# Optimization experiments

Measured on AMD Instinct MI355X. Metric: run time of the kernel, lower is better.

Reference implementation:

```python
import math
import jax, jax.numpy as jnp
import numpy as np

L, F, K = 3, 128, 20          # layers, hidden size, rbf size
CUTOFF = 5.0
B, NPER, EPER = 4, 4096, 49152  # graphs, nodes/graph, edges/graph
NVOC = 119                    # len(ase.data.atomic_numbers)
PNAMES = ['atom_emb','pot_W','pot_b','init_W1','init_b1','init_W2','init_b2','vec_w',
          'filt_W','filt_b','msg_W1','msg_b1','msg_W2','msg_b2','U_W','V_W',
          'upd_W1','upd_b1','upd_W2','upd_b2']


def _painn(atom_xyz, cell, nodes, atom_edges, edges_displacement, V_flat, E_flat, p):
    N = B * NPER
    pos = atom_xyz.reshape(N, 3)
    # edge_offset = cumsum(num_nodes) ; all graphs have NPER nodes
    off = (jnp.arange(B, dtype=atom_edges.dtype) * NPER)[:, None, None]
    edges = (atom_edges + off).reshape(B * EPER, 2)
    # calc_distance with periodic cell offsets
    disp = jnp.einsum('bec,bcd->bed', edges_displacement, cell).reshape(B * EPER, 3)
    send, recv = edges[:, 0], edges[:, 1]
    diff = pos[recv] - (pos[send] + disp)                       # [E,3]
    dist = jnp.sqrt(jnp.sum(diff * diff, axis=1, keepdims=True))  # [E,1]
    # sinc RBF expansion
    n_range = jnp.arange(1, K + 1, dtype=jnp.float32)
    edge_state = jnp.sin(dist * n_range * (math.pi / CUTOFF)) / dist  # [E,K]
    # init scalar features: Embedding(Z) || Linear(V) -> MLP
    s_atom = p['atom_emb'][nodes.reshape(N)]                    # [N,F]
    s_pot = V_flat @ p['pot_W'].T + p['pot_b']                  # [N,F]
    h = jnp.concatenate([s_atom, s_pot], axis=-1)
    s = jax.nn.silu(h @ p['init_W1'].T + p['init_b1']) @ p['init_W2'].T + p['init_b2']  # [N,F]
    # init vector features: no-bias Linear(1->F) on E field
    v = E_flat[:, :, None] * p['vec_w']                         # [N,3,F]
    cut = jnp.where(dist < CUTOFF, 0.5 * (jnp.cos(math.pi * dist / CUTOFF) + 1.0), 0.0)  # [E,1]
    dirn = diff / jnp.maximum(dist, 1e-12)                      # [E,3]
    s_list, v_list = [], []
    for l in range(L):
        # --- PaiNNInteraction ---
        fw = (edge_state @ p['filt_W'][l].T + p['filt_b'][l]) * cut                # [E,3F]
        so = jax.nn.silu(s @ p['msg_W1'][l].T + p['msg_b1'][l]) @ p['msg_W2'][l].T + p['msg_b2'][l]  # [N,3F]
        fo = fw * so[send]                                                          # [E,3F]
        g_sv, g_ev, g_ns = jnp.split(fo, 3, axis=1)
        msg_s = s[send] * g_ns                                                      # [E,F]
        msg_v = v[send] * g_sv[:, None, :] + g_ev[:, None, :] * dirn[:, :, None]    # [E,3,F]
        s = s + jax.ops.segment_sum(msg_s, recv, num_segments=N)
        v = v + jax.ops.segment_sum(msg_v, recv, num_segments=N)
        # --- PaiNNUpdate ---
        Uv = v @ p['U_W'][l].T                                                      # [N,3,F]
        Vv = v @ p['V_W'][l].T                                                      # [N,3,F]
        Vn = jnp.sqrt(jnp.sum(Vv * Vv, axis=1))                                     # [N,F]
        m = jnp.concatenate([s, Vn], axis=1)
        m = jax.nn.silu(m @ p['upd_W1'][l].T + p['upd_b1'][l]) @ p['upd_W2'][l].T + p['upd_b2'][l]
        a_ss, a_sv, a_vv = jnp.split(m, 3, axis=1)
        s = s + a_ss + a_sv * jnp.sum(Uv * Vv, axis=1)
        v = v + a_vv[:, None, :] * Uv
        s_list.append(s)
        v_list.append(v)
    # pack trajectory: [L,N,1,F] scalar || [L,N,3,F] vector -> [L,N,4,F]
    return jnp.concatenate([jnp.stack(s_list)[:, :, None, :], jnp.stack(v_list)], axis=2)


def setup_inputs() -> dict:
    key = jax.random.key(0)
    ks = iter(jax.random.split(key, 48))
    def nrm(shape, scale=0.05):
        return jax.random.normal(next(ks), shape, dtype=jnp.float32) * scale
    atom_xyz = jax.random.uniform(next(ks), (B, NPER, 3), dtype=jnp.float32) * 30.0
    cell = jnp.tile(jnp.eye(3, dtype=jnp.float32)[None] * 30.0, (B, 1, 1))
    nodes = jax.random.randint(next(ks), (B, NPER), 0, NVOC)
    e0 = jax.random.randint(next(ks), (B, EPER), 0, NPER)
    delta = jax.random.randint(next(ks), (B, EPER), 1, NPER)
    e1 = (e0 + delta) % NPER  # sender != receiver -> no zero-distance edges
    atom_edges = jnp.stack([e0, e1], axis=-1)
    edges_displacement = jax.random.randint(next(ks), (B, EPER, 3), -1, 2).astype(jnp.float32)
    V_flat = nrm((B * NPER, 1), 1.0)
    E_flat = nrm((B * NPER, 3), 1.0)
    params = dict(
        atom_emb=nrm((NVOC, F), 1.0),
        pot_W=nrm((F, 1)), pot_b=nrm((F,)),
        init_W1=nrm((F, 2 * F)), init_b1=nrm((F,)),
        init_W2=nrm((F, F)), init_b2=nrm((F,)),
        vec_w=nrm((F,)),
        filt_W=nrm((L, 3 * F, K)), filt_b=nrm((L, 3 * F)),
        msg_W1=nrm((L, F, F)), msg_b1=nrm((L, F)),
        msg_W2=nrm((L, 3 * F, F)), msg_b2=nrm((L, 3 * F)),
        U_W=nrm((L, F, F)), V_W=nrm((L, F, F)),
        upd_W1=nrm((L, F, 2 * F)), upd_b1=nrm((L, F)),
        upd_W2=nrm((L, 3 * F, F)), upd_b2=nrm((L, 3 * F)),
    )
    return dict(atom_xyz=atom_xyz, cell=cell, nodes=nodes, atom_edges=atom_edges,
                edges_displacement=edges_displacement, V_flat=V_flat, E_flat=E_flat, **params)


def reference(atom_xyz, cell, nodes, atom_edges, edges_displacement, V_flat, E_flat,
              atom_emb, pot_W, pot_b, init_W1, init_b1, init_W2, init_b2, vec_w,
              filt_W, filt_b, msg_W1, msg_b1, msg_W2, msg_b2, U_W, V_W,
              upd_W1, upd_b1, upd_W2, upd_b2):
    p = dict(zip(PNAMES, (atom_emb, pot_W, pot_b, init_W1, init_b1, init_W2, init_b2, vec_w,
                          filt_W, filt_b, msg_W1, msg_b1, msg_W2, msg_b2, U_W, V_W,
                          upd_W1, upd_b1, upd_W2, upd_b2)))
    return _painn(atom_xyz, cell, nodes, atom_edges, edges_displacement, V_flat, E_flat, p)
```

## Files before the change

### kernel.cpp

```cpp
#include <hip/hip_runtime.h>
#include <math.h>

#define NPER  4096
#define NTOT  16384
#define EPER  49152
#define ETOT  196608
#define FD    128
#define F3    384
#define KR    20
#define PI_F  3.14159265358979f
#define PADF  132

typedef unsigned short u16;
typedef __attribute__((ext_vector_type(8))) short s16x8;
typedef __attribute__((ext_vector_type(4))) float f32x4;
typedef _Float16 h16x2 __attribute__((ext_vector_type(2)));
typedef _Float16 h16x4 __attribute__((ext_vector_type(4)));
typedef _Float16 h16x8 __attribute__((ext_vector_type(8)));

#if defined(__has_builtin)
#if __has_builtin(__builtin_amdgcn_fdot2)
#define FDOT2(a,b,c) __builtin_amdgcn_fdot2((a),(b),(c),false)
#endif
#endif
#ifndef FDOT2
#define FDOT2(a,b,c) ((float)(a)[0]*(float)(b)[0] + (float)(a)[1]*(float)(b)[1] + (c))
#endif

__device__ __forceinline__ float silu_f(float x){ return x / (1.0f + __expf(-x)); }
__device__ __forceinline__ u16 f2b(float x){
    unsigned u = __float_as_uint(x);
    u = u + 0x7FFFu + ((u >> 16) & 1u);
    return (u16)(u >> 16);
}
__device__ __forceinline__ float b2f(u16 h){ return __uint_as_float(((unsigned)h) << 16); }

struct __align__(16) EdgeRec {
    float4 ed;
    h16x8  es0;
    h16x8  es1;
    h16x4  es2;
    h16x4  pad;
};

__global__ __launch_bounds__(256) void ecount_kernel(
    const int* __restrict__ aedges, int* __restrict__ counts)
{
    int e = blockIdx.x * blockDim.x + threadIdx.x;
    if (e >= ETOT) return;
    int r = aedges[(size_t)e*2+1] + (e / EPER)*NPER;
    atomicAdd(&counts[r],1);
}

__global__ __launch_bounds__(1024) void scan_kernel(const int* __restrict__ counts,
                                                    int* __restrict__ row_off)
{
    __shared__ int sdata[1024];
    int t = threadIdx.x;
    int base = t * 16;
    int local[16];
    int s = 0;
    #pragma unroll
    for (int i=0;i<16;++i){ local[i]=s; s += counts[base+i]; }
    sdata[t] = s;
    __syncthreads();
    for (int off=1; off<1024; off<<=1) {
        int val = (t>=off) ? sdata[t-off] : 0;
        __syncthreads();
        sdata[t] += val;
        __syncthreads();
    }
    int chunk_off = (t==0) ? 0 : sdata[t-1];
    #pragma unroll
    for (int i=0;i<16;++i) row_off[base+i] = chunk_off + local[i];
    if (t==1023) row_off[NTOT] = sdata[1023];
}

__global__ __launch_bounds__(256) void fill_kernel(
    const float* __restrict__ xyz, const float* __restrict__ cell,
    const int* __restrict__ aedges, const float* __restrict__ edisp,
    const int* __restrict__ row_off, int* __restrict__ cursor,
    int* __restrict__ sd_csr, EdgeRec* __restrict__ erec_csr)
{
    int e = blockIdx.x * blockDim.x + threadIdx.x;
    if (e >= ETOT) return;
    int b = e / EPER;
    int s = aedges[(size_t)e*2+0] + b*NPER;
    int r = aedges[(size_t)e*2+1] + b*NPER;
    const float* cb = cell + b*9;
    float c0 = edisp[(size_t)e*3+0], c1 = edisp[(size_t)e*3+1], c2 = edisp[(size_t)e*3+2];
    float diff[3];
    #pragma unroll
    for (int d=0; d<3; ++d) {
        float disp = c0*cb[d] + c1*cb[3+d] + c2*cb[6+d];
        diff[d] = xyz[(size_t)r*3+d] - (xyz[(size_t)s*3+d] + disp);
    }
    float dist = sqrtf(diff[0]*diff[0]+diff[1]*diff[1]+diff[2]*diff[2]);
    float cut = (dist < 5.0f) ? 0.5f*(__cosf(PI_F*dist*0.2f)+1.0f) : 0.0f;
    float invg = 1.0f/fmaxf(dist,1e-12f);
    EdgeRec rec;
    rec.ed = make_float4(diff[0]*invg, diff[1]*invg, diff[2]*invg, cut);
    float theta = dist*(PI_F*0.2f);
    float s1 = __sinf(theta), cth = __cosf(theta);
    float scale = cut / dist;
    float twoc = 2.f*cth;
    float sm1 = 0.f, sk = s1;
    _Float16 esv[20];
    #pragma unroll
    for (int k=0;k<20;++k){
        esv[k] = (_Float16)(sk*scale);
        float nx = twoc*sk - sm1;
        sm1 = sk; sk = nx;
    }
    union { h16x8 v; _Float16 h[8]; } u0, u1;
    union { h16x4 v; _Float16 h[4]; } u2;
    #pragma unroll
    for (int i=0;i<8;++i){ u0.h[i]=esv[i]; u1.h[i]=esv[8+i]; }
    #pragma unroll
    for (int i=0;i<4;++i) u2.h[i]=esv[16+i];
    rec.es0=u0.v; rec.es1=u1.v; rec.es2=u2.v;
    rec.pad = (h16x4)((_Float16)0);
    int slot = atomicAdd(&cursor[r], 1);
    int pos = row_off[r] + slot;
    sd_csr[pos] = s;
    erec_csr[pos] = rec;
}

__global__ __launch_bounds__(256) void wconv_kernel(
    const float* __restrict__ w0, const float* __restrict__ w1,
    const float* __restrict__ w2, const float* __restrict__ w3,
    const float* __restrict__ w4, const float* __restrict__ w5,
    const float* __restrict__ w6, const float* __restrict__ w7,
    u16* __restrict__ dst)
{
    int t = blockIdx.x*256 + threadIdx.x;
    if (t >= 589824) return;
    const float* src; int off; int d = t;
    if      (t < 32768)  { src=w0; off=t; }
    else if (t < 49152)  { src=w1; off=t-32768; }
    else if (t < 98304)  { src=w2; off=t-49152; }
    else if (t < 245760) { src=w3; off=t-98304; }
    else if (t < 294912) { int o=t-245760; int l=o>>14; int r=o&16383; src=w4; off=o;
                           d = 245760 + l*32768 + r; }
    else if (t < 344064) { int o=t-294912; int l=o>>14; int r=o&16383; src=w5; off=o;
                           d = 245760 + l*32768 + 16384 + r; }
    else if (t < 442368) { src=w6; off=t-344064; }
    else                 { src=w7; off=t-442368; }
    dst[d] = f2b(src[off]);
}

__global__ __launch_bounds__(256) void wfilt_kernel(const float* __restrict__ fW,
                                                    _Float16* __restrict__ dst)
{
    int t = blockIdx.x*256 + threadIdx.x;
    if (t < 3*F3*KR) dst[t] = (_Float16)fW[t];
}

__global__ __launch_bounds__(256) void hbuild_kernel(const int* __restrict__ nodes,
    const float* __restrict__ atom_emb, const float* __restrict__ V_flat,
    const float* __restrict__ pot_W, const float* __restrict__ pot_b,
    u16* __restrict__ h)
{
    int t = blockIdx.x * blockDim.x + threadIdx.x;
    int n = t >> 8, k = t & 255;
    float val;
    if (k < FD) val = atom_emb[(size_t)nodes[n]*FD + k];
    else { int f = k - FD; val = V_flat[n]*pot_W[f] + pot_b[f]; }
    h[t] = f2b(val);
}

__global__ __launch_bounds__(256) void v0_kernel(const float* __restrict__ E_flat,
    const float* __restrict__ vec_w, float* __restrict__ v0, u16* __restrict__ vq)
{
    int t = blockIdx.x * blockDim.x + threadIdx.x;
    int n = t / F3, r = t - n*F3;
    int c = r >> 7, f = r & 127;
    float val = E_flat[(size_t)n*3 + c] * vec_w[f];
    v0[t] = val;
    vq[((size_t)n*FD + f)*4 + c] = f2b(val);
}

template<int ACT>
__global__ __launch_bounds__(256) void bgemm_kernel(
    const u16* __restrict__ A, int lda,
    const u16* __restrict__ W, int Kdim,
    const float* __restrict__ bias,
    float* __restrict__ C, int ldc,
    u16* __restrict__ Cb, int ldcb,
    u16* __restrict__ Cq, int qoff)
{
    const int tid  = threadIdx.x;
    const int wave = tid >> 6, lane = tid & 63;
    const int q = lane >> 4, im = lane & 15;
    const int row0 = blockIdx.y*64 + wave*16;
    const int col0 = blockIdx.x*64;
    f32x4 acc[4];
    #pragma unroll
    for (int n=0;n<4;++n) acc[n] = (f32x4){0.f,0.f,0.f,0.f};
    const u16* Ap = A + (size_t)(row0+im)*lda + q*8;
    const u16* Wp = W + (size_t)(col0+im)*Kdim + q*8;
    for (int k0 = 0; k0 < Kdim; k0 += 32) {
        s16x8 af = *(const s16x8*)(Ap + k0);
        #pragma unroll
        for (int n=0;n<4;++n) {
            s16x8 bf = *(const s16x8*)(Wp + (size_t)n*16*Kdim + k0);
            acc[n] = __builtin_amdgcn_mfma_f32_16x16x32_bf16(af, bf, acc[n], 0, 0, 0);
        }
    }
    #pragma unroll
    for (int n=0;n<4;++n) {
        int col = col0 + n*16 + im;
        float bv = bias ? bias[col] : 0.f;
        #pragma unroll
        for (int r=0;r<4;++r) {
            int row = row0 + q*4 + r;
            float v = acc[n][r] + bv;
            if (ACT) v = silu_f(v);
            if (C)  C[(size_t)row*ldc + col] = v;
            if (Cb) Cb[(size_t)row*ldcb + col] = f2b(v);
            if (Cq) Cq[((size_t)row*FD + (col & 127))*4 + (col >> 7) + qoff] = f2b(v);
        }
    }
}

#define HID_OFF(row, col2b) ((unsigned)((row)*256 + (col2b)*2) ^ ((unsigned)((row)&7) << 4))
#define M_OFF(row, col2b)   ((unsigned)((row)*512 + (col2b)*2) ^ ((unsigned)((row)&7) << 4))

__global__ __launch_bounds__(256) void msgmlp_kernel(
    const u16* __restrict__ A,
    const u16* __restrict__ W1,
    const float* __restrict__ b1,
    const u16* __restrict__ W2,
    const float* __restrict__ b2,
    u16* __restrict__ sq)
{
    __shared__ u16 hid[16*FD];
    const int tid = threadIdx.x;
    const int wave = tid >> 6, lane = tid & 63;
    const int q = lane >> 4, im = lane & 15;
    const int row0 = blockIdx.x * 16;
    {
        f32x4 acc[2];
        #pragma unroll
        for (int n=0;n<2;++n) acc[n] = (f32x4){0.f,0.f,0.f,0.f};
        const u16* Ap = A + (size_t)(row0+im)*FD + q*8;
        #pragma unroll
        for (int k0=0;k0<FD;k0+=32) {
            s16x8 af = *(const s16x8*)(Ap + k0);
            #pragma unroll
            for (int n=0;n<2;++n) {
                s16x8 bf = *(const s16x8*)(W1 + (size_t)(wave*32+n*16+im)*FD + k0 + q*8);
                acc[n] = __builtin_amdgcn_mfma_f32_16x16x32_bf16(af, bf, acc[n], 0, 0, 0);
            }
        }
        #pragma unroll
        for (int n=0;n<2;++n) {
            int col = wave*32 + n*16 + im;
            float bv = b1[col];
            #pragma unroll
            for (int r=0;r<4;++r) {
                int row = q*4 + r;
                *(u16*)((char*)hid + HID_OFF(row, col)) = f2b(silu_f(acc[n][r]+bv));
            }
        }
    }
    __syncthreads();
    s16x8 af[4];
    #pragma unroll
    for (int k=0;k<4;++k)
        af[k] = *(const s16x8*)((char*)hid + HID_OFF(im, k*32+q*8));
    #pragma unroll
    for (int jj=0;jj<2;++jj) {
        int j = wave*2 + jj;
        f32x4 a2[3];
        #pragma unroll
        for (int g=0;g<3;++g) a2[g] = (f32x4){0.f,0.f,0.f,0.f};
        #pragma unroll
        for (int k=0;k<4;++k) {
            #pragma unroll
            for (int g=0;g<3;++g) {
                s16x8 bf = *(const s16x8*)(W2 + (size_t)(g*128 + j*16 + im)*FD + k*32 + q*8);
                a2[g] = __builtin_amdgcn_mfma_f32_16x16x32_bf16(af[k], bf, a2[g], 0, 0, 0);
            }
        }
        int fcol = j*16 + im;
        float c0 = b2[fcol], c1 = b2[FD+fcol], c2 = b2[2*FD+fcol];
        #pragma unroll
        for (int r=0;r<4;++r) {
            int row = row0 + q*4 + r;
            size_t t4 = ((size_t)row*FD + fcol)*4;
            unsigned pk = (unsigned)f2b(a2[0][r]+c0) | ((unsigned)f2b(a2[1][r]+c1) << 16);
            *(unsigned*)(sq + t4) = pk;
            sq[t4+2] = f2b(a2[2][r]+c2);
        }
    }
}

__global__ __launch_bounds__(256) void upduv_kernel(
    const u16* __restrict__ vmid4,
    const u16* __restrict__ Wuv,
    const u16* __restrict__ W1,
    const float* __restrict__ b1,
    const u16* __restrict__ W2,
    const float* __restrict__ b2,
    const float* __restrict__ s_mid, const float* __restrict__ v_mid,
    float* __restrict__ outp, u16* __restrict__ s_bf,
    u16* __restrict__ sq, u16* __restrict__ vq)
{
    __shared__ u16   mL[16*256];
    __shared__ float dotL[16*PADF];
    __shared__ float uvL[48*PADF];
    __shared__ u16   hid[16*FD];
    const int tid = threadIdx.x;
    const int wave = tid >> 6, lane = tid & 63;
    const int q = lane >> 4, im = lane & 15;
    const int node0 = blockIdx.x * 16;

    {
        const int prow0 = blockIdx.x*64 + wave*16;
        const u16* Ap = vmid4 + (size_t)(prow0+im)*FD + q*8;
        s16x8 af[4];
        #pragma unroll
        for (int k=0;k<4;++k) af[k] = *(const s16x8*)(Ap + k*32);
        const int nloc = wave*4 + q;
        #pragma unroll
        for (int j=0;j<8;++j) {
            f32x4 aU = (f32x4){0.f,0.f,0.f,0.f};
            f32x4 aV = (f32x4){0.f,0.f,0.f,0.f};
            const u16* WpU = Wuv + (size_t)(j*16+im)*FD + q*8;
            const u16* WpV = WpU + (size_t)128*FD;
            #pragma unroll
            for (int k=0;k<4;++k) {
                s16x8 bU = *(const s16x8*)(WpU + k*32);
                s16x8 bV = *(const s16x8*)(WpV + k*32);
                aU = __builtin_amdgcn_mfma_f32_16x16x32_bf16(af[k], bU, aU, 0, 0, 0);
                aV = __builtin_amdgcn_mfma_f32_16x16x32_bf16(af[k], bV, aV, 0, 0, 0);
            }
            int fcol = j*16 + im;
            float u0=aU[0], u1=aU[1], u2=aU[2];
            float w0=aV[0], w1=aV[1], w2=aV[2];
            dotL[nloc*PADF + fcol] = u0*w0 + u1*w1 + u2*w2;
            *(u16*)((char*)mL + M_OFF(nloc, 128+fcol)) = f2b(sqrtf(w0*w0+w1*w1+w2*w2));
            uvL[(nloc*3+0)*PADF + fcol] = u0;
            uvL[(nloc*3+1)*PADF + fcol] = u1;
            uvL[(nloc*3+2)*PADF + fcol] = u2;
        }
    }
    {
        int row = tid >> 4;
        int c0  = (tid & 15) * 8;
        const float* sp = s_mid + (size_t)(node0+row)*FD + c0;
        union { s16x8 v; u16 h[8]; } pk;
        #pragma unroll
        for (int i=0;i<8;++i) pk.h[i] = f2b(sp[i]);
        *(s16x8*)((char*)mL + M_OFF(row, c0)) = pk.v;
    }
    __syncthreads();
    {
        f32x4 acc[2];
        #pragma unroll
        for (int n=0;n<2;++n) acc[n] = (f32x4){0.f,0.f,0.f,0.f};
        #pragma unroll
        for (int k0=0;k0<256;k0+=32) {
            s16x8 af = *(const s16x8*)((char*)mL + M_OFF(im, k0+q*8));
            #pragma unroll
            for (int n=0;n<2;++n) {
                s16x8 bf = *(const s16x8*)(W1 + (size_t)(wave*32+n*16+im)*256 + k0 + q*8);
                acc[n] = __builtin_amdgcn_mfma_f32_16x16x32_bf16(af, bf, acc[n], 0, 0, 0);
            }
        }
        #pragma unroll
        for (int n=0;n<2;++n) {
            int col = wave*32 + n*16 + im;
            float bv = b1[col];
            #pragma unroll
            for (int r=0;r<4;++r) {
                int row = q*4 + r;
                *(u16*)((char*)hid + HID_OFF(row, col)) = f2b(silu_f(acc[n][r]+bv));
            }
        }
    }
    __syncthreads();
    s16x8 af2[4];
    #pragma unroll
    for (int k=0;k<4;++k)
        af2[k] = *(const s16x8*)((char*)hid + HID_OFF(im, k*32+q*8));
    #pragma unroll
    for (int jj=0;jj<2;++jj) {
        int j = wave*2 + jj;
        f32x4 a2[3];
        #pragma unroll
        for (int g=0;g<3;++g) a2[g] = (f32x4){0.f,0.f,0.f,0.f};
        #pragma unroll
        for (int k=0;k<4;++k) {
            #pragma unroll
            for (int g=0;g<3;++g) {
                s16x8 bf = *(const s16x8*)(W2 + (size_t)(g*128 + j*16 + im)*FD + k*32 + q*8);
                a2[g] = __builtin_amdgcn_mfma_f32_16x16x32_bf16(af2[k], bf, a2[g], 0, 0, 0);
            }
        }
        int fcol = j*16 + im;
        float b_ss = b2[fcol], b_sv = b2[FD+fcol], b_vv = b2[2*FD+fcol];
        #pragma unroll
        for (int r=0;r<4;++r) {
            int rl = q*4 + r;
            int row = node0 + rl;
            float a_ss = a2[0][r] + b_ss;
            float a_sv = a2[1][r] + b_sv;
            float a_vv = a2[2][r] + b_vv;
            size_t t = (size_t)row*FD + fcol;
            float sval = s_mid[t] + a_ss + a_sv*dotL[rl*PADF + fcol];
            outp[(size_t)row*512 + fcol] = sval;
            s_bf[t] = f2b(sval);
            sq[t*4 + 3] = f2b(sval);
            ushort4 pack;
            #pragma unroll
            for (int c=0;c<3;++c) {
                size_t vi = ((size_t)row*3 + c)*FD + fcol;
                float vval = v_mid[vi] + a_vv*uvL[(rl*3+c)*PADF + fcol];
                outp[(size_t)row*512 + (1+c)*FD + fcol] = vval;
                ((u16*)&pack)[c] = f2b(vval);
            }
            ((u16*)&pack)[3] = 0;
            *(ushort4*)(vq + t*4) = pack;
        }
    }
}

__device__ __forceinline__ void edge_step(
    const EdgeRec& er, ushort4 s4, ushort4 v4,
    const h16x2* wp,
    float b0, float b1, float b2,
    float& acc_s, float& av0, float& av1, float& av2)
{
    union { h16x8 v; h16x2 p[4]; } e0, e1;
    union { h16x4 v; h16x2 p[2]; } e2;
    e0.v = er.es0; e1.v = er.es1; e2.v = er.es2;
    h16x2 ep[10] = {e0.p[0],e0.p[1],e0.p[2],e0.p[3],
                    e1.p[0],e1.p[1],e1.p[2],e1.p[3],
                    e2.p[0],e2.p[1]};
    float4 ed = er.ed;
    float d0=0.f, d1=0.f, d2=0.f;
    #pragma unroll
    for (int j=0;j<10;++j){
        d0 = FDOT2(ep[j], wp[j],    d0);
        d1 = FDOT2(ep[j], wp[10+j], d1);
        d2 = FDOT2(ep[j], wp[20+j], d2);
    }
    float g_sv = d0 + b0*ed.w;
    float g_ev = d1 + b1*ed.w;
    float g_ns = d2 + b2*ed.w;
    float fo_sv = g_sv * b2f(s4.x);
    float fo_ev = g_ev * b2f(s4.y);
    float fo_ns = g_ns * b2f(s4.z);
    acc_s += b2f(s4.w) * fo_ns;
    av0 += b2f(v4.x)*fo_sv + fo_ev*ed.x;
    av1 += b2f(v4.y)*fo_sv + fo_ev*ed.y;
    av2 += b2f(v4.z)*fo_sv + fo_ev*ed.z;
}

__global__ __launch_bounds__(256) __attribute__((amdgpu_waves_per_eu(4,8)))
void agg_kernel(
    const float* __restrict__ s_prev_f, int s_ldaf,
    const float* __restrict__ v_prev_f, int v_nstrf,
    const ushort4* __restrict__ sq, const ushort4* __restrict__ vq,
    const EdgeRec* __restrict__ erec_csr,
    const int* __restrict__ sd_csr, const int* __restrict__ row_off,
    const _Float16* __restrict__ wf, const float* __restrict__ fb,
    float* __restrict__ s_mid, float* __restrict__ v_mid,
    u16* __restrict__ vmid4_bf)
{
    const int f   = threadIdx.x & 127;
    const int sub = threadIdx.x >> 7;
    h16x2 wp[30];
    #pragma unroll
    for (int rsel=0; rsel<3; ++rsel){
        const h16x4* rp = (const h16x4*)(wf + (size_t)(rsel*FD + f)*KR);
        #pragma unroll
        for (int i=0;i<5;++i){
            union { h16x4 v; h16x2 p[2]; } t; t.v = rp[i];
            wp[rsel*10+2*i]   = t.p[0];
            wp[rsel*10+2*i+1] = t.p[1];
        }
    }
    const float b0 = fb[f], b1 = fb[FD+f], b2 = fb[2*FD+f];

    const int n = blockIdx.x*2 + sub;
    const int beg = __builtin_amdgcn_readfirstlane(row_off[n]);
    const int end = __builtin_amdgcn_readfirstlane(row_off[n+1]);
    float acc_s=0.f, av0=0.f, av1=0.f, av2=0.f;

    int i0 = (beg   < end) ? beg   : 0;
    int i1 = (beg+1 < end) ? beg+1 : i0;
    int sd0 = __builtin_amdgcn_readfirstlane(sd_csr[i0]);
    int sd1 = __builtin_amdgcn_readfirstlane(sd_csr[i1]);
    ushort4 sA = sq[(size_t)sd0*FD + f];
    ushort4 vA = vq[(size_t)sd0*FD + f];
    ushort4 sB = sq[(size_t)sd1*FD + f];
    ushort4 vB = vq[(size_t)sd1*FD + f];
    EdgeRec r0 = erec_csr[i0];
    EdgeRec r1 = erec_csr[i1];

    for (int idx = beg; idx + 2 <= end; idx += 2) {
        int j0 = (idx+2 < end) ? idx+2 : 0;
        int j1 = (idx+3 < end) ? idx+3 : j0;
        int nsd0 = __builtin_amdgcn_readfirstlane(sd_csr[j0]);
        int nsd1 = __builtin_amdgcn_readfirstlane(sd_csr[j1]);
        ushort4 nsA = sq[(size_t)nsd0*FD + f];
        ushort4 nvA = vq[(size_t)nsd0*FD + f];
        ushort4 nsB = sq[(size_t)nsd1*FD + f];
        ushort4 nvB = vq[(size_t)nsd1*FD + f];
        EdgeRec nr0 = erec_csr[j0];
        EdgeRec nr1 = erec_csr[j1];

        edge_step(r0, sA, vA, wp, b0,b1,b2, acc_s, av0, av1, av2);
        edge_step(r1, sB, vB, wp, b0,b1,b2, acc_s, av0, av1, av2);

        sA=nsA; vA=nvA; sB=nsB; vB=nvB; r0=nr0; r1=nr1;
    }
    if (((end - beg) & 1) && beg < end) {
        edge_step(r0, sA, vA, wp, b0,b1,b2, acc_s, av0, av1, av2);
    }

    float smv = s_prev_f[(size_t)n*s_ldaf+f] + acc_s;
    s_mid[(size_t)n*FD+f] = smv;
    const float* vp = v_prev_f + (size_t)n*v_nstrf;
    float o0 = vp[f]+av0, o1 = vp[FD+f]+av1, o2 = vp[2*FD+f]+av2;
    size_t vo = (size_t)n*F3;
    v_mid[vo+f]=o0;        v_mid[vo+FD+f]=o1;        v_mid[vo+2*FD+f]=o2;
    size_t v4 = (size_t)n*512;
    vmid4_bf[v4+f]=f2b(o0); vmid4_bf[v4+FD+f]=f2b(o1); vmid4_bf[v4+2*FD+f]=f2b(o2);
}

extern "C" void kernel_launch(void* const* d_in, const int* in_sizes, int n_in,
                              void* d_out, int out_size, void* d_ws, size_t ws_size,
                              hipStream_t stream)
{
    (void)in_sizes; (void)n_in; (void)out_size; (void)ws_size;
    const float* atom_xyz = (const float*)d_in[0];
    const float* cell     = (const float*)d_in[1];
    const int*   nodes    = (const int*)d_in[2];
    const int*   aedges   = (const int*)d_in[3];
    const float* edisp    = (const float*)d_in[4];
    const float* V_flat   = (const float*)d_in[5];
    const float* E_flat   = (const float*)d_in[6];
    const float* atom_emb = (const float*)d_in[7];
    const float* pot_W    = (const float*)d_in[8];
    const float* pot_b    = (const float*)d_in[9];
    const float* init_W1  = (const float*)d_in[10];
    const float* init_b1  = (const float*)d_in[11];
    const float* init_W2  = (const float*)d_in[12];
    const float* init_b2  = (const float*)d_in[13];
    const float* vec_w    = (const float*)d_in[14];
    const float* filt_W   = (const float*)d_in[15];
    const float* filt_b   = (const float*)d_in[16];
    const float* msg_W1   = (const float*)d_in[17];
    const float* msg_b1   = (const float*)d_in[18];
    const float* msg_W2   = (const float*)d_in[19];
    const float* msg_b2   = (const float*)d_in[20];
    const float* U_W      = (const float*)d_in[21];
    const float* V_W      = (const float*)d_in[22];
    const float* upd_W1   = (const float*)d_in[23];
    const float* upd_b1   = (const float*)d_in[24];
    const float* upd_W2   = (const float*)d_in[25];
    const float* upd_b2   = (const float*)d_in[26];

    float* out = (float*)d_out;
    char* base = (char*)d_ws;
    size_t o = 0;
    auto alloc = [&](size_t bytes)->char* { char* r = base + o; o += (bytes + 255) & ~(size_t)255; return r; };

    float* s0     = (float*)alloc((size_t)NTOT*FD*4);
    float* v0     = (float*)alloc((size_t)NTOT*F3*4);
    float* s_mid  = (float*)alloc((size_t)NTOT*FD*4);
    float* v_mid  = (float*)alloc((size_t)NTOT*F3*4);
    EdgeRec* erec_csr = (EdgeRec*)alloc((size_t)ETOT*sizeof(EdgeRec));
    u16* h_bf     = (u16*)alloc((size_t)NTOT*256*2);
    u16* s_bf     = (u16*)alloc((size_t)NTOT*FD*2);
    u16* sq       = (u16*)alloc((size_t)NTOT*FD*4*2);
    u16* vq       = (u16*)alloc((size_t)NTOT*FD*4*2);
    u16* hid_bf   = (u16*)alloc((size_t)NTOT*FD*2);
    u16* vmid4_bf = (u16*)alloc((size_t)NTOT*4*FD*2);
    u16* wts      = (u16*)alloc((size_t)589824*2);
    _Float16* wf16 = (_Float16*)alloc((size_t)3*F3*KR*2);
    int* sd_csr   = (int*)alloc((size_t)ETOT*4);
    int* row_off  = (int*)alloc((size_t)(NTOT+1)*4);
    int* counts   = (int*)alloc((size_t)NTOT*4);
    int* cursor   = (int*)alloc((size_t)NTOT*4);

    hipMemsetAsync(counts, 0, NTOT*sizeof(int), stream);
    hipMemsetAsync(cursor, 0, NTOT*sizeof(int), stream);
    hipMemsetAsync(vmid4_bf, 0, (size_t)NTOT*4*FD*2, stream);

    ecount_kernel<<<ETOT/256, 256, 0, stream>>>(aedges, counts);
    scan_kernel<<<1, 1024, 0, stream>>>(counts, row_off);
    fill_kernel<<<ETOT/256, 256, 0, stream>>>(atom_xyz, cell, aedges, edisp,
        row_off, cursor, sd_csr, erec_csr);
    wconv_kernel<<<(589824+255)/256, 256, 0, stream>>>(
        init_W1, init_W2, msg_W1, msg_W2, U_W, V_W, upd_W1, upd_W2, wts);
    wfilt_kernel<<<(3*F3*KR+255)/256, 256, 0, stream>>>(filt_W, wf16);

    const u16* w_init1 = wts + 0;
    const u16* w_init2 = wts + 32768;
    const u16* w_msg1  = wts + 49152;
    const u16* w_msg2  = wts + 98304;
    const u16* w_UV    = wts + 245760;
    const u16* w_upd1  = wts + 344064;
    const u16* w_upd2  = wts + 442368;

    hbuild_kernel<<<NTOT*256/256, 256, 0, stream>>>(nodes, atom_emb, V_flat, pot_W, pot_b, h_bf);
    bgemm_kernel<1><<<dim3(FD/64, NTOT/64), 256, 0, stream>>>(
        h_bf, 256, w_init1, 256, init_b1, (float*)nullptr, 0, hid_bf, FD, (u16*)nullptr, 0);
    bgemm_kernel<0><<<dim3(FD/64, NTOT/64), 256, 0, stream>>>(
        hid_bf, FD, w_init2, FD, init_b2, s0, FD, s_bf, FD, sq, 3);
    v0_kernel<<<NTOT*F3/256, 256, 0, stream>>>(E_flat, vec_w, v0, vq);

    const float* s_prev_f = s0;  int s_ldaf  = FD;
    const float* v_prev_f = v0;  int v_nstrf = 3*FD;
    for (int l = 0; l < 3; ++l) {
        msgmlp_kernel<<<NTOT/16, 256, 0, stream>>>(
            s_bf, w_msg1 + (size_t)l*16384, msg_b1 + (size_t)l*FD,
            w_msg2 + (size_t)l*49152, msg_b2 + (size_t)l*F3, sq);
        agg_kernel<<<NTOT/2, 256, 0, stream>>>(s_prev_f, s_ldaf, v_prev_f, v_nstrf,
            (const ushort4*)sq, (const ushort4*)vq, erec_csr, sd_csr, row_off,
            wf16 + (size_t)l*F3*KR, filt_b + (size_t)l*F3, s_mid, v_mid, vmid4_bf);
        float* outp = out + (size_t)l*NTOT*512;
        upduv_kernel<<<NTOT/16, 256, 0, stream>>>(
            vmid4_bf, w_UV + (size_t)l*32768,
            w_upd1 + (size_t)l*32768, upd_b1 + (size_t)l*FD,
            w_upd2 + (size_t)l*49152, upd_b2 + (size_t)l*F3,
            s_mid, v_mid, outp, s_bf, sq, vq);
        s_prev_f = outp;        s_ldaf  = 512;
        v_prev_f = outp + FD;   v_nstrf = 512;
    }
}
```

Baseline: 658.4 us.

## Shrink upduv LDS with XOR swizzle, reuse mL for hidden, remap edge blocks

In the update kernel, the padded dotL/uvL shared arrays become unpadded arrays with an XOR swizzle that keeps bank conflicts low, and the hidden activation buffer now reuses the mL buffer behind an extra barrier. Together these cut LDS use per block, so more blocks can be resident. The message-passing kernel also remaps block IDs so that blocks in consecutive dispatch order handle nodes spread across graphs, which is meant to improve cache locality or load balance across XCDs. The cost is one more __syncthreads and extra address arithmetic.

```diff
diff --git a/kernel.cpp b/kernel.cpp
--- a/kernel.cpp
+++ b/kernel.cpp
@@ -9,7 +9,6 @@
 #define F3    384
 #define KR    20
 #define PI_F  3.14159265358979f
-#define PADF  132
 
 typedef unsigned short u16;
 typedef __attribute__((ext_vector_type(8))) short s16x8;
@@ -225,6 +224,7 @@
 
 #define HID_OFF(row, col2b) ((unsigned)((row)*256 + (col2b)*2) ^ ((unsigned)((row)&7) << 4))
 #define M_OFF(row, col2b)   ((unsigned)((row)*512 + (col2b)*2) ^ ((unsigned)((row)&7) << 4))
+#define DK(row) (((((unsigned)(row))&1u)^((((unsigned)(row))>>2)&1u))<<6)
 
 __global__ __launch_bounds__(256) void msgmlp_kernel(
     const u16* __restrict__ A,
@@ -308,9 +308,8 @@
     u16* __restrict__ sq, u16* __restrict__ vq)
 {
     __shared__ u16   mL[16*256];
-    __shared__ float dotL[16*PADF];
-    __shared__ float uvL[48*PADF];
-    __shared__ u16   hid[16*FD];
+    __shared__ float dotL[16*128];
+    __shared__ float uvL[3*16*128];
     const int tid = threadIdx.x;
     const int wave = tid >> 6, lane = tid & 63;
     const int q = lane >> 4, im = lane & 15;
@@ -339,11 +338,12 @@
             int fcol = j*16 + im;
             float u0=aU[0], u1=aU[1], u2=aU[2];
             float w0=aV[0], w1=aV[1], w2=aV[2];
-            dotL[nloc*PADF + fcol] = u0*w0 + u1*w1 + u2*w2;
+            *(float*)((char*)dotL + (((unsigned)(nloc*512 + fcol*4)) ^ DK(nloc))) =
+                u0*w0 + u1*w1 + u2*w2;
             *(u16*)((char*)mL + M_OFF(nloc, 128+fcol)) = f2b(sqrtf(w0*w0+w1*w1+w2*w2));
-            uvL[(nloc*3+0)*PADF + fcol] = u0;
-            uvL[(nloc*3+1)*PADF + fcol] = u1;
-            uvL[(nloc*3+2)*PADF + fcol] = u2;
+            *(float*)((char*)uvL + (((unsigned)(0*8192 + nloc*512 + fcol*4)) ^ DK(nloc))) = u0;
+            *(float*)((char*)uvL + (((unsigned)(1*8192 + nloc*512 + fcol*4)) ^ DK(nloc))) = u1;
+            *(float*)((char*)uvL + (((unsigned)(2*8192 + nloc*512 + fcol*4)) ^ DK(nloc))) = u2;
         }
     }
     {
@@ -356,28 +356,28 @@
         *(s16x8*)((char*)mL + M_OFF(row, c0)) = pk.v;
     }
     __syncthreads();
-    {
-        f32x4 acc[2];
-        #pragma unroll
-        for (int n=0;n<2;++n) acc[n] = (f32x4){0.f,0.f,0.f,0.f};
-        #pragma unroll
-        for (int k0=0;k0<256;k0+=32) {
-            s16x8 af = *(const s16x8*)((char*)mL + M_OFF(im, k0+q*8));
-            #pragma unroll
-            for (int n=0;n<2;++n) {
-                s16x8 bf = *(const s16x8*)(W1 + (size_t)(wave*32+n*16+im)*256 + k0 + q*8);
-                acc[n] = __builtin_amdgcn_mfma_f32_16x16x32_bf16(af, bf, acc[n], 0, 0, 0);
-            }
-        }
+    f32x4 acc1[2];
+    #pragma unroll
+    for (int n=0;n<2;++n) acc1[n] = (f32x4){0.f,0.f,0.f,0.f};
+    #pragma unroll
+    for (int k0=0;k0<256;k0+=32) {
+        s16x8 af = *(const s16x8*)((char*)mL + M_OFF(im, k0+q*8));
         #pragma unroll
         for (int n=0;n<2;++n) {
-            int col = wave*32 + n*16 + im;
-            float bv = b1[col];
-            #pragma unroll
-            for (int r=0;r<4;++r) {
-                int row = q*4 + r;
-                *(u16*)((char*)hid + HID_OFF(row, col)) = f2b(silu_f(acc[n][r]+bv));
-            }
+            s16x8 bf = *(const s16x8*)(W1 + (size_t)(wave*32+n*16+im)*256 + k0 + q*8);
+            acc1[n] = __builtin_amdgcn_mfma_f32_16x16x32_bf16(af, bf, acc1[n], 0, 0, 0);
+        }
+    }
+    __syncthreads();
+    u16* hid = mL;
+    #pragma unroll
+    for (int n=0;n<2;++n) {
+        int col = wave*32 + n*16 + im;
+        float bv = b1[col];
+        #pragma unroll
+        for (int r=0;r<4;++r) {
+            int row = q*4 + r;
+            *(u16*)((char*)hid + HID_OFF(row, col)) = f2b(silu_f(acc1[n][r]+bv));
         }
     }
     __syncthreads();
@@ -409,7 +409,9 @@
             float a_sv = a2[1][r] + b_sv;
             float a_vv = a2[2][r] + b_vv;
             size_t t = (size_t)row*FD + fcol;
-            float sval = s_mid[t] + a_ss + a_sv*dotL[rl*PADF + fcol];
+            float dotv = *(const float*)((char*)dotL +
+                             (((unsigned)(rl*512 + fcol*4)) ^ DK(rl)));
+            float sval = s_mid[t] + a_ss + a_sv*dotv;
             outp[(size_t)row*512 + fcol] = sval;
             s_bf[t] = f2b(sval);
             sq[t*4 + 3] = f2b(sval);
@@ -417,7 +419,9 @@
             #pragma unroll
             for (int c=0;c<3;++c) {
                 size_t vi = ((size_t)row*3 + c)*FD + fcol;
-                float vval = v_mid[vi] + a_vv*uvL[(rl*3+c)*PADF + fcol];
+                float uvv = *(const float*)((char*)uvL +
+                               (((unsigned)(c*8192 + rl*512 + fcol*4)) ^ DK(rl)));
+                float vval = v_mid[vi] + a_vv*uvv;
                 outp[(size_t)row*512 + (1+c)*FD + fcol] = vval;
                 ((u16*)&pack)[c] = f2b(vval);
             }
@@ -485,7 +489,9 @@
     }
     const float b0 = fb[f], b1 = fb[FD+f], b2 = fb[2*FD+f];
 
-    const int n = blockIdx.x*2 + sub;
+    const int bsw = blockIdx.x;
+    const int nb  = ((bsw & 7) >> 1)*2048 + (bsw & 1)*1024 + (bsw >> 3);
+    const int n = nb*2 + sub;
     const int beg = __builtin_amdgcn_readfirstlane(row_off[n]);
     const int end = __builtin_amdgcn_readfirstlane(row_off[n+1]);
     float acc_s=0.f, av0=0.f, av1=0.f, av2=0.f;
```

New measurement: 690.3 us. 1.05x slower.

## Fuse init embedding build and two-layer init MLP into one kernel; recompute v0 in agg

Applied to the files above, without the earlier changes.

Replaces the h-build kernel and the two bgemm launches for the initial scalar MLP with a single hinit kernel. It builds the embedding/potential row tile in shared memory and runs both GEMMs with the hidden layer staged in LDS. The fp32 v0 buffer is dropped; the layer-0 aggregation recomputes E_flat*vec_w on the fly instead of reading it. This removes two launches and several global round trips of intermediates, at the cost of a 16-row-per-block GEMM that rereads weights from global more often.

```diff
diff --git a/kernel.cpp b/kernel.cpp
--- a/kernel.cpp
+++ b/kernel.cpp
@@ -156,75 +156,99 @@
     if (t < 3*F3*KR) dst[t] = (_Float16)fW[t];
 }
 
-__global__ __launch_bounds__(256) void hbuild_kernel(const int* __restrict__ nodes,
-    const float* __restrict__ atom_emb, const float* __restrict__ V_flat,
-    const float* __restrict__ pot_W, const float* __restrict__ pot_b,
-    u16* __restrict__ h)
-{
-    int t = blockIdx.x * blockDim.x + threadIdx.x;
-    int n = t >> 8, k = t & 255;
-    float val;
-    if (k < FD) val = atom_emb[(size_t)nodes[n]*FD + k];
-    else { int f = k - FD; val = V_flat[n]*pot_W[f] + pot_b[f]; }
-    h[t] = f2b(val);
-}
-
 __global__ __launch_bounds__(256) void v0_kernel(const float* __restrict__ E_flat,
-    const float* __restrict__ vec_w, float* __restrict__ v0, u16* __restrict__ vq)
+    const float* __restrict__ vec_w, u16* __restrict__ vq)
 {
     int t = blockIdx.x * blockDim.x + threadIdx.x;
     int n = t / F3, r = t - n*F3;
     int c = r >> 7, f = r & 127;
-    float val = E_flat[(size_t)n*3 + c] * vec_w[f];
-    v0[t] = val;
-    vq[((size_t)n*FD + f)*4 + c] = f2b(val);
-}
-
-template<int ACT>
-__global__ __launch_bounds__(256) void bgemm_kernel(
-    const u16* __restrict__ A, int lda,
-    const u16* __restrict__ W, int Kdim,
-    const float* __restrict__ bias,
-    float* __restrict__ C, int ldc,
-    u16* __restrict__ Cb, int ldcb,
-    u16* __restrict__ Cq, int qoff)
-{
-    const int tid  = threadIdx.x;
+    vq[((size_t)n*FD + f)*4 + c] = f2b(E_flat[(size_t)n*3 + c] * vec_w[f]);
+}
+
+#define HID_OFF(row, col2b) ((unsigned)((row)*256 + (col2b)*2) ^ ((unsigned)((row)&7) << 4))
+#define M_OFF(row, col2b)   ((unsigned)((row)*512 + (col2b)*2) ^ ((unsigned)((row)&7) << 4))
+
+__global__ __launch_bounds__(256) void hinit_kernel(
+    const int* __restrict__ nodes,
+    const float* __restrict__ atom_emb, const float* __restrict__ V_flat,
+    const float* __restrict__ pot_W, const float* __restrict__ pot_b,
+    const u16* __restrict__ W1,
+    const float* __restrict__ b1,
+    const u16* __restrict__ W2,
+    const float* __restrict__ b2,
+    float* __restrict__ s0, u16* __restrict__ s_bf, u16* __restrict__ sq)
+{
+    __shared__ u16 mL[16*256];
+    __shared__ u16 hid[16*FD];
+    const int tid = threadIdx.x;
     const int wave = tid >> 6, lane = tid & 63;
     const int q = lane >> 4, im = lane & 15;
-    const int row0 = blockIdx.y*64 + wave*16;
-    const int col0 = blockIdx.x*64;
-    f32x4 acc[4];
-    #pragma unroll
-    for (int n=0;n<4;++n) acc[n] = (f32x4){0.f,0.f,0.f,0.f};
-    const u16* Ap = A + (size_t)(row0+im)*lda + q*8;
-    const u16* Wp = W + (size_t)(col0+im)*Kdim + q*8;
-    for (int k0 = 0; k0 < Kdim; k0 += 32) {
-        s16x8 af = *(const s16x8*)(Ap + k0);
-        #pragma unroll
-        for (int n=0;n<4;++n) {
-            s16x8 bf = *(const s16x8*)(Wp + (size_t)n*16*Kdim + k0);
-            acc[n] = __builtin_amdgcn_mfma_f32_16x16x32_bf16(af, bf, acc[n], 0, 0, 0);
-        }
-    }
-    #pragma unroll
-    for (int n=0;n<4;++n) {
-        int col = col0 + n*16 + im;
-        float bv = bias ? bias[col] : 0.f;
+    const int row0 = blockIdx.x * 16;
+    {
+        int row = tid >> 4;
+        int c0  = (tid & 15) * 16;
+        int nid = nodes[row0 + row];
+        float vf = V_flat[row0 + row];
+        #pragma unroll
+        for (int i=0;i<16;++i) {
+            int col = c0 + i;
+            float val = (col < FD) ? atom_emb[(size_t)nid*FD + col]
+                                   : vf * pot_W[col-FD] + pot_b[col-FD];
+            *(u16*)((char*)mL + M_OFF(row, col)) = f2b(val);
+        }
+    }
+    __syncthreads();
+    {
+        f32x4 acc[2];
+        #pragma unroll
+        for (int n=0;n<2;++n) acc[n] = (f32x4){0.f,0.f,0.f,0.f};
+        #pragma unroll
+        for (int k0=0;k0<256;k0+=32) {
+            s16x8 af = *(const s16x8*)((char*)mL + M_OFF(im, k0+q*8));
+            #pragma unroll
+            for (int n=0;n<2;++n) {
+                s16x8 bf = *(const s16x8*)(W1 + (size_t)(wave*32+n*16+im)*256 + k0 + q*8);
+                acc[n] = __builtin_amdgcn_mfma_f32_16x16x32_bf16(af, bf, acc[n], 0, 0, 0);
+            }
+        }
+        #pragma unroll
+        for (int n=0;n<2;++n) {
+            int col = wave*32 + n*16 + im;
+            float bv = b1[col];
+            #pragma unroll
+            for (int r=0;r<4;++r) {
+                int row = q*4 + r;
+                *(u16*)((char*)hid + HID_OFF(row, col)) = f2b(silu_f(acc[n][r]+bv));
+            }
+        }
+    }
+    __syncthreads();
+    s16x8 af2[4];
+    #pragma unroll
+    for (int k=0;k<4;++k)
+        af2[k] = *(const s16x8*)((char*)hid + HID_OFF(im, k*32+q*8));
+    #pragma unroll
+    for (int jj=0;jj<2;++jj) {
+        int j = wave*2 + jj;
+        f32x4 a2 = (f32x4){0.f,0.f,0.f,0.f};
+        #pragma unroll
+        for (int k=0;k<4;++k) {
+            s16x8 bf = *(const s16x8*)(W2 + (size_t)(j*16 + im)*FD + k*32 + q*8);
+            a2 = __builtin_amdgcn_mfma_f32_16x16x32_bf16(af2[k], bf, a2, 0, 0, 0);
+        }
+        int fcol = j*16 + im;
+        float bv = b2[fcol];
         #pragma unroll
         for (int r=0;r<4;++r) {
             int row = row0 + q*4 + r;
-            float v = acc[n][r] + bv;
-            if (ACT) v = silu_f(v);
-            if (C)  C[(size_t)row*ldc + col] = v;
-            if (Cb) Cb[(size_t)row*ldcb + col] = f2b(v);
-            if (Cq) Cq[((size_t)row*FD + (col & 127))*4 + (col >> 7) + qoff] = f2b(v);
-        }
-    }
-}
-
-#define HID_OFF(row, col2b) ((unsigned)((row)*256 + (col2b)*2) ^ ((unsigned)((row)&7) << 4))
-#define M_OFF(row, col2b)   ((unsigned)((row)*512 + (col2b)*2) ^ ((unsigned)((row)&7) << 4))
+            float v = a2[r] + bv;
+            size_t t = (size_t)row*FD + fcol;
+            s0[t] = v;
+            s_bf[t] = f2b(v);
+            sq[t*4 + 3] = f2b(v);
+        }
+    }
+}
 
 __global__ __launch_bounds__(256) void msgmlp_kernel(
     const u16* __restrict__ A,
@@ -468,7 +492,8 @@
     const int* __restrict__ sd_csr, const int* __restrict__ row_off,
     const _Float16* __restrict__ wf, const float* __restrict__ fb,
     float* __restrict__ s_mid, float* __restrict__ v_mid,
-    u16* __restrict__ vmid4_bf)
+    u16* __restrict__ vmid4_bf,
+    const float* __restrict__ E_flat, const float* __restrict__ vec_w, int l0)
 {
     const int f   = threadIdx.x & 127;
     const int sub = threadIdx.x >> 7;
@@ -524,8 +549,18 @@
 
     float smv = s_prev_f[(size_t)n*s_ldaf+f] + acc_s;
     s_mid[(size_t)n*FD+f] = smv;
-    const float* vp = v_prev_f + (size_t)n*v_nstrf;
-    float o0 = vp[f]+av0, o1 = vp[FD+f]+av1, o2 = vp[2*FD+f]+av2;
+    float base0, base1, base2;
+    if (l0) {
+        float e0 = E_flat[(size_t)n*3+0];
+        float e1 = E_flat[(size_t)n*3+1];
+        float e2 = E_flat[(size_t)n*3+2];
+        float vw = vec_w[f];
+        base0 = e0*vw; base1 = e1*vw; base2 = e2*vw;
+    } else {
+        const float* vp = v_prev_f + (size_t)n*v_nstrf;
+        base0 = vp[f]; base1 = vp[FD+f]; base2 = vp[2*FD+f];
+    }
+    float o0 = base0+av0, o1 = base1+av1, o2 = base2+av2;
     size_t vo = (size_t)n*F3;
     v_mid[vo+f]=o0;        v_mid[vo+FD+f]=o1;        v_mid[vo+2*FD+f]=o2;
     size_t v4 = (size_t)n*512;
@@ -571,15 +606,12 @@
     auto alloc = [&](size_t bytes)->char* { char* r = base + o; o += (bytes + 255) & ~(size_t)255; return r; };
 
     float* s0     = (float*)alloc((size_t)NTOT*FD*4);
-    float* v0     = (float*)alloc((size_t)NTOT*F3*4);
     float* s_mid  = (float*)alloc((size_t)NTOT*FD*4);
     float* v_mid  = (float*)alloc((size_t)NTOT*F3*4);
     EdgeRec* erec_csr = (EdgeRec*)alloc((size_t)ETOT*sizeof(EdgeRec));
-    u16* h_bf     = (u16*)alloc((size_t)NTOT*256*2);
     u16* s_bf     = (u16*)alloc((size_t)NTOT*FD*2);
     u16* sq       = (u16*)alloc((size_t)NTOT*FD*4*2);
     u16* vq       = (u16*)alloc((size_t)NTOT*FD*4*2);
-    u16* hid_bf   = (u16*)alloc((size_t)NTOT*FD*2);
     u16* vmid4_bf = (u16*)alloc((size_t)NTOT*4*FD*2);
     u16* wts      = (u16*)alloc((size_t)589824*2);
     _Float16* wf16 = (_Float16*)alloc((size_t)3*F3*KR*2);
@@ -608,22 +640,21 @@
     const u16* w_upd1  = wts + 344064;
     const u16* w_upd2  = wts + 442368;
 
-    hbuild_kernel<<<NTOT*256/256, 256, 0, stream>>>(nodes, atom_emb, V_flat, pot_W, pot_b, h_bf);
-    bgemm_kernel<1><<<dim3(FD/64, NTOT/64), 256, 0, stream>>>(
-        h_bf, 256, w_init1, 256, init_b1, (float*)nullptr, 0, hid_bf, FD, (u16*)nullptr, 0);
-    bgemm_kernel<0><<<dim3(FD/64, NTOT/64), 256, 0, stream>>>(
-        hid_bf, FD, w_init2, FD, init_b2, s0, FD, s_bf, FD, sq, 3);
-    v0_kernel<<<NTOT*F3/256, 256, 0, stream>>>(E_flat, vec_w, v0, vq);
+    hinit_kernel<<<NTOT/16, 256, 0, stream>>>(
+        nodes, atom_emb, V_flat, pot_W, pot_b,
+        w_init1, init_b1, w_init2, init_b2, s0, s_bf, sq);
+    v0_kernel<<<NTOT*F3/256, 256, 0, stream>>>(E_flat, vec_w, vq);
 
     const float* s_prev_f = s0;  int s_ldaf  = FD;
-    const float* v_prev_f = v0;  int v_nstrf = 3*FD;
+    const float* v_prev_f = s0;  int v_nstrf = 0;
     for (int l = 0; l < 3; ++l) {
         msgmlp_kernel<<<NTOT/16, 256, 0, stream>>>(
             s_bf, w_msg1 + (size_t)l*16384, msg_b1 + (size_t)l*FD,
             w_msg2 + (size_t)l*49152, msg_b2 + (size_t)l*F3, sq);
         agg_kernel<<<NTOT/2, 256, 0, stream>>>(s_prev_f, s_ldaf, v_prev_f, v_nstrf,
             (const ushort4*)sq, (const ushort4*)vq, erec_csr, sd_csr, row_off,
-            wf16 + (size_t)l*F3*KR, filt_b + (size_t)l*F3, s_mid, v_mid, vmid4_bf);
+            wf16 + (size_t)l*F3*KR, filt_b + (size_t)l*F3, s_mid, v_mid, vmid4_bf,
+            E_flat, vec_w, l == 0 ? 1 : 0);
         float* outp = out + (size_t)l*NTOT*512;
         upduv_kernel<<<NTOT/16, 256, 0, stream>>>(
             vmid4_bf, w_UV + (size_t)l*32768,
```

Result: no change. 645.7 us (-1.9%).
